# Kernel tuning notes

Measured on AMD Instinct MI355X. Metric: run time of the kernel, lower is better.

## Reference

```python
import jax, jax.numpy as jnp
import numpy as np

B, S, D, H, DH = 4, 2048, 1024, 16, 64

def setup_inputs() -> dict:
    key = jax.random.key(0)
    k1, k2, k3, k4, k5 = jax.random.split(key, 5)
    scale = 1.0 / np.sqrt(D)
    return {
        "x": jax.random.normal(k1, (B, S, D), dtype=jnp.float32),
        "w_qkv": jax.random.normal(k2, (D, 3, H, DH), dtype=jnp.float32) * scale,
        "b_qkv": jax.random.normal(k3, (3, H, DH), dtype=jnp.float32) * 0.02,
        "w_out": jax.random.normal(k4, (H, DH, D), dtype=jnp.float32) * (1.0 / np.sqrt(H * DH)),
        "b_out": jax.random.normal(k5, (D,), dtype=jnp.float32) * 0.02,
    }

def reference(x, w_qkv, b_qkv, w_out, b_out):
    # QKV projection: [B,S,D] x [D,3,H,Dh] -> [B,S,3,H,Dh]
    qkv = jnp.einsum('bsd,dthe->bsthe', x, w_qkv) + b_qkv
    q, k, v = qkv[:, :, 0], qkv[:, :, 1], qkv[:, :, 2]  # each [B,S,H,Dh]
    head_dim = q.shape[-1]
    # scores [B,H,Sq,Sk]
    scores = jnp.einsum('bqhe,bkhe->bhqk', q, k) / jnp.sqrt(jnp.float32(head_dim))
    seq = scores.shape[-1]
    causal = (jnp.arange(seq)[:, None] >= jnp.arange(seq)[None, :]).astype(scores.dtype)
    scores = scores - 1e9 * (1.0 - causal)  # additive mask as in source
    weights = jax.nn.softmax(scores, axis=-1)
    # dropout inactive (inference=True default)
    answers = jnp.einsum('bhqk,bkhe->bqhe', weights, v)  # [B,S,H,Dh]
    out = jnp.einsum('bqhe,hed->bqd', answers, w_out) + b_out
    return out
```

## Files before the change

kernel.cpp:

```cpp
#include <hip/hip_runtime.h>
#include <hip/hip_bf16.h>
#include <stdint.h>

#define B_    4
#define S_    2048
#define D_    1024
#define H_    16
#define DH_   64
#define M_TOT 8192
#define NQKV  3072
#define HDH   1024

typedef __bf16 bf16_t;
typedef bf16_t bf16x8 __attribute__((ext_vector_type(8)));
typedef float  f32x4  __attribute__((ext_vector_type(4)));
typedef float  f32x16 __attribute__((ext_vector_type(16)));

#define QSCALE 0.1803368801111204f

__device__ __forceinline__ short f2bf(float f) {
  union { float f; uint32_t u; } x; x.f = f;
  uint32_t r = (x.u + 0x7fffu + ((x.u >> 16) & 1u)) >> 16;
  return (short)(uint16_t)r;
}

__device__ __forceinline__ uint32_t cvt_pk_bf16(float lo, float hi) {
  uint32_t r;
  asm("v_cvt_pk_bf16_f32 %0, %1, %2" : "=v"(r) : "v"(lo), "v"(hi));
  return r;
}

__device__ __forceinline__ void permlane32_swap(uint32_t& d, uint32_t& s) {
  asm("v_permlane32_swap_b32 %0, %1" : "+v"(d), "+v"(s));
}

#define ASYNC_COPY16(g, l) \
  __builtin_amdgcn_global_load_lds((const __attribute__((address_space(1))) void*)(g), \
                                   (__attribute__((address_space(3))) void*)(l), 16, 0, 0)


__global__ __launch_bounds__(256) void k_cvt(const float* __restrict__ in, short* __restrict__ out, int n4) {
  int i = blockIdx.x * 256 + threadIdx.x;
  if (i < n4) {
    float4 v = ((const float4*)in)[i];
    short4 o;
    o.x = f2bf(v.x); o.y = f2bf(v.y); o.z = f2bf(v.z); o.w = f2bf(v.w);
    ((short4*)out)[i] = o;
  }
}

__global__ __launch_bounds__(256) void k_transpose_t(const float* __restrict__ in, short* __restrict__ out,
                                                     int R, int C) {
  __shared__ short t[32][33];
  const int bx = blockIdx.x * 32;
  const int by = blockIdx.y * 32;
  const int tid = threadIdx.x;
  const int row = tid >> 3, c4 = (tid & 7) * 4;
  const float4 v = *(const float4*)&in[(size_t)(by + row) * C + bx + c4];
  t[row][c4 + 0] = f2bf(v.x); t[row][c4 + 1] = f2bf(v.y);
  t[row][c4 + 2] = f2bf(v.z); t[row][c4 + 3] = f2bf(v.w);
  __syncthreads();
  short4 o;
  o.x = t[c4 + 0][row]; o.y = t[c4 + 1][row];
  o.z = t[c4 + 2][row]; o.w = t[c4 + 3][row];
  *(short4*)&out[(size_t)(bx + row) * R + by + c4] = o;
}


__device__ __forceinline__ void gemm_core(const short* __restrict__ A,
                                          const short* __restrict__ Bt,
                                          int row0, int col0, int K,
                                          short* lA, short* lB,
                                          f32x4 acc[4][4]) {
  const int tid  = threadIdx.x;
  const int wave = tid >> 6, lane = tid & 63;
  const int wr = wave >> 1, wc = wave & 1;
  const int stg_r = lane >> 2;
  const int stg_k = (lane & 3) * 8;
  const int fr = lane & 15;
  const int fk = (lane >> 4) * 8;

  for (int k0 = 0; k0 < K; k0 += 32) {
    __syncthreads();
#pragma unroll
    for (int c = 0; c < 2; ++c) {
      const int seg = wave * 2 + c;
      const short* ga = A  + (size_t)(row0 + seg * 16 + stg_r) * K + (k0 + stg_k);
      const short* gb = Bt + (size_t)(col0 + seg * 16 + stg_r) * K + (k0 + stg_k);
      ASYNC_COPY16(ga, lA + seg * 512);
      ASYNC_COPY16(gb, lB + seg * 512);
    }
    __syncthreads();
    bf16x8 af[4], bfr[4];
#pragma unroll
    for (int m = 0; m < 4; ++m)
      af[m] = *(const bf16x8*)(lA + (wr * 64 + m * 16 + fr) * 32 + fk);
#pragma unroll
    for (int n = 0; n < 4; ++n)
      bfr[n] = *(const bf16x8*)(lB + (wc * 64 + n * 16 + fr) * 32 + fk);
#pragma unroll
    for (int m = 0; m < 4; ++m)
#pragma unroll
      for (int n = 0; n < 4; ++n)
        acc[m][n] = __builtin_amdgcn_mfma_f32_16x16x32_bf16(af[m], bfr[n], acc[m][n], 0, 0, 0);
  }
}

__global__ __launch_bounds__(256) void k_gemm_qkv(const short* __restrict__ A, const short* __restrict__ Bt,
                                                  const float* __restrict__ bias,
                                                  short* __restrict__ Qb, short* __restrict__ Kb,
                                                  short* __restrict__ Vt) {
  __shared__ short lA[128 * 32];
  __shared__ short lB[128 * 32];
  f32x4 acc[4][4];
#pragma unroll
  for (int m = 0; m < 4; ++m)
#pragma unroll
    for (int n = 0; n < 4; ++n)
      acc[m][n] = (f32x4){0.f, 0.f, 0.f, 0.f};
  const int row0 = blockIdx.x * 128, col0 = blockIdx.y * 128;
  gemm_core(A, Bt, row0, col0, D_, lA, lB, acc);
  const int lane = threadIdx.x & 63, wave = threadIdx.x >> 6;
  const int wr = wave >> 1, wc = wave & 1;
#pragma unroll
  for (int m = 0; m < 4; ++m) {
    const int rbase = row0 + wr * 64 + m * 16 + (lane >> 4) * 4;
    const int bb = rbase >> 11, s0 = rbase & 2047;
#pragma unroll
    for (int n = 0; n < 4; ++n) {
      const int col = col0 + wc * 64 + n * 16 + (lane & 15);
      const float bv = bias[col];
      const int t = col >> 10, rem = col & 1023, hh = rem >> 6, e = rem & 63;
      if (t == 2) {
        short4 o;
        o.x = f2bf(acc[m][n][0] + bv);
        o.y = f2bf(acc[m][n][1] + bv);
        o.z = f2bf(acc[m][n][2] + bv);
        o.w = f2bf(acc[m][n][3] + bv);
        *(short4*)&Vt[((size_t)(bb * H_ + hh) * DH_ + e) * S_ + s0] = o;
      } else if (t == 0) {
#pragma unroll
        for (int r = 0; r < 4; ++r)
          Qb[((size_t)(bb * H_ + hh) * S_ + (s0 + r)) * DH_ + e] = f2bf((acc[m][n][r] + bv) * QSCALE);
      } else {
#pragma unroll
        for (int r = 0; r < 4; ++r)
          Kb[((size_t)(bb * H_ + hh) * S_ + (s0 + r)) * DH_ + e] = f2bf(acc[m][n][r] + bv);
      }
    }
  }
}

__global__ __launch_bounds__(256) void k_gemm_out(const short* __restrict__ A, const short* __restrict__ Bt,
                                                  const float* __restrict__ bias, float* __restrict__ C) {
  __shared__ short lA[128 * 32];
  __shared__ short lB[128 * 32];
  f32x4 acc[4][4];
#pragma unroll
  for (int m = 0; m < 4; ++m)
#pragma unroll
    for (int n = 0; n < 4; ++n)
      acc[m][n] = (f32x4){0.f, 0.f, 0.f, 0.f};
  const int row0 = blockIdx.x * 128, col0 = blockIdx.y * 128;
  gemm_core(A, Bt, row0, col0, HDH, lA, lB, acc);
  const int lane = threadIdx.x & 63, wave = threadIdx.x >> 6;
  const int wr = wave >> 1, wc = wave & 1;
#pragma unroll
  for (int m = 0; m < 4; ++m) {
    const int rbase = row0 + wr * 64 + m * 16 + (lane >> 4) * 4;
#pragma unroll
    for (int n = 0; n < 4; ++n) {
      const int col = col0 + wc * 64 + n * 16 + (lane & 15);
      const float bv = bias[col];
#pragma unroll
      for (int r = 0; r < 4; ++r)
        C[(size_t)(rbase + r) * D_ + col] = acc[m][n][r] + bv;
    }
  }
}


template <bool MASKED>
__device__ __forceinline__ void softmax_pack(const f32x16& sacc, int ql, int hi,
                                             f32x16& o0, f32x16& o1,
                                             float& m, float& lsum,
                                             bf16x8& pb0v, bf16x8& pb1v) {
  float p[16];
#pragma unroll
  for (int r = 0; r < 16; ++r) {
    float s = sacc[r];
    if (MASKED) {
      const int kl = (r & 3) + 8 * (r >> 2) + 4 * hi;
      s = (kl <= ql) ? s : -1.0e30f;
    }
    p[r] = s;
  }
  float t0 = fmaxf(fmaxf(p[0], p[1]), p[2]);
  float t1 = fmaxf(fmaxf(p[3], p[4]), p[5]);
  float t2 = fmaxf(fmaxf(p[6], p[7]), p[8]);
  float t3 = fmaxf(fmaxf(p[9], p[10]), p[11]);
  float t4 = fmaxf(fmaxf(p[12], p[13]), p[14]);
  float pmax = fmaxf(fmaxf(fmaxf(t0, t1), t2), fmaxf(fmaxf(t3, t4), p[15]));
  if (__any(pmax - m > 8.0f)) {
    const float pmr = fmaxf(pmax, __shfl_xor(pmax, 32));
    const float mn = fmaxf(m, pmr);
    const float al = __builtin_amdgcn_exp2f(m - mn);
    lsum *= al;
#pragma unroll
    for (int r = 0; r < 16; ++r) { o0[r] *= al; o1[r] *= al; }
    m = mn;
  }
#pragma unroll
  for (int r = 0; r < 16; ++r) p[r] = __builtin_amdgcn_exp2f(p[r] - m);
  {
    float s0 = (p[0] + p[1]) + (p[2] + p[3]);
    float s1 = (p[4] + p[5]) + (p[6] + p[7]);
    float s2 = (p[8] + p[9]) + (p[10] + p[11]);
    float s3 = (p[12] + p[13]) + (p[14] + p[15]);
    lsum += (s0 + s1) + (s2 + s3);
  }
  uint32_t A0 = cvt_pk_bf16(p[0],  p[1]);
  uint32_t A1 = cvt_pk_bf16(p[2],  p[3]);
  uint32_t B0 = cvt_pk_bf16(p[4],  p[5]);
  uint32_t B1 = cvt_pk_bf16(p[6],  p[7]);
  uint32_t A2 = cvt_pk_bf16(p[8],  p[9]);
  uint32_t A3 = cvt_pk_bf16(p[10], p[11]);
  uint32_t B2 = cvt_pk_bf16(p[12], p[13]);
  uint32_t B3 = cvt_pk_bf16(p[14], p[15]);
  permlane32_swap(A0, B0);
  permlane32_swap(A1, B1);
  permlane32_swap(A2, B2);
  permlane32_swap(A3, B3);
  union { uint32_t u[4]; bf16x8 v; } pb0, pb1;
  pb0.u[0] = A0; pb0.u[1] = A1; pb0.u[2] = B0; pb0.u[3] = B1;
  pb1.u[0] = A2; pb1.u[1] = A3; pb1.u[2] = B2; pb1.u[3] = B3;
  pb0v = pb0.v; pb1v = pb1.v;
}

template <bool MASKED>
__device__ __forceinline__ void attn_tile(int kt, int ql, int hi,
                                          const short* __restrict__ Kp,
                                          const short* __restrict__ Vp,
                                          const bf16x8 qf[4],
                                          f32x16& oacc0, f32x16& oacc1,
                                          float& m, float& lsum) {
  const short* kb = Kp + (size_t)(kt + ql) * DH_ + hi * 8;
  bf16x8 kf0 = *(const bf16x8*)(kb);
  bf16x8 kf1 = *(const bf16x8*)(kb + 16);
  bf16x8 kf2 = *(const bf16x8*)(kb + 32);
  bf16x8 kf3 = *(const bf16x8*)(kb + 48);
  const short* vb0 = Vp + (size_t)(ql) * S_ + kt + hi * 8;
  const short* vb1 = Vp + (size_t)(32 + ql) * S_ + kt + hi * 8;
  bf16x8 vf00 = *(const bf16x8*)(vb0);
  bf16x8 vf01 = *(const bf16x8*)(vb0 + 16);
  bf16x8 vf10 = *(const bf16x8*)(vb1);
  bf16x8 vf11 = *(const bf16x8*)(vb1 + 16);

  f32x16 sacc;
#pragma unroll
  for (int r = 0; r < 16; ++r) sacc[r] = 0.f;
  __builtin_amdgcn_s_setprio(1);
  sacc = __builtin_amdgcn_mfma_f32_32x32x16_bf16(kf0, qf[0], sacc, 0, 0, 0);
  sacc = __builtin_amdgcn_mfma_f32_32x32x16_bf16(kf1, qf[1], sacc, 0, 0, 0);
  sacc = __builtin_amdgcn_mfma_f32_32x32x16_bf16(kf2, qf[2], sacc, 0, 0, 0);
  sacc = __builtin_amdgcn_mfma_f32_32x32x16_bf16(kf3, qf[3], sacc, 0, 0, 0);
  __builtin_amdgcn_s_setprio(0);

  bf16x8 pb0, pb1;
  softmax_pack<MASKED>(sacc, ql, hi, oacc0, oacc1, m, lsum, pb0, pb1);

  __builtin_amdgcn_s_setprio(1);
  oacc0 = __builtin_amdgcn_mfma_f32_32x32x16_bf16(vf00, pb0, oacc0, 0, 0, 0);
  oacc0 = __builtin_amdgcn_mfma_f32_32x32x16_bf16(vf01, pb1, oacc0, 0, 0, 0);
  oacc1 = __builtin_amdgcn_mfma_f32_32x32x16_bf16(vf10, pb0, oacc1, 0, 0, 0);
  oacc1 = __builtin_amdgcn_mfma_f32_32x32x16_bf16(vf11, pb1, oacc1, 0, 0, 0);
  __builtin_amdgcn_s_setprio(0);
}

template <bool MASKA>
__device__ __forceinline__ void attn_tile2(int kt, int ql, int hi,
                                           const short* __restrict__ Kp,
                                           const short* __restrict__ Vp,
                                           const bf16x8 qfA[4], const bf16x8 qfB[4],
                                           f32x16& oA0, f32x16& oA1, float& mA, float& lA,
                                           f32x16& oB0, f32x16& oB1, float& mB, float& lB) {
  const short* kb = Kp + (size_t)(kt + ql) * DH_ + hi * 8;
  bf16x8 kf0 = *(const bf16x8*)(kb);
  bf16x8 kf1 = *(const bf16x8*)(kb + 16);
  bf16x8 kf2 = *(const bf16x8*)(kb + 32);
  bf16x8 kf3 = *(const bf16x8*)(kb + 48);
  const short* vb0 = Vp + (size_t)(ql) * S_ + kt + hi * 8;
  const short* vb1 = Vp + (size_t)(32 + ql) * S_ + kt + hi * 8;
  bf16x8 vf00 = *(const bf16x8*)(vb0);
  bf16x8 vf01 = *(const bf16x8*)(vb0 + 16);
  bf16x8 vf10 = *(const bf16x8*)(vb1);
  bf16x8 vf11 = *(const bf16x8*)(vb1 + 16);

  f32x16 sA, sB;
#pragma unroll
  for (int r = 0; r < 16; ++r) { sA[r] = 0.f; sB[r] = 0.f; }
  __builtin_amdgcn_s_setprio(1);
  sA = __builtin_amdgcn_mfma_f32_32x32x16_bf16(kf0, qfA[0], sA, 0, 0, 0);
  sB = __builtin_amdgcn_mfma_f32_32x32x16_bf16(kf0, qfB[0], sB, 0, 0, 0);
  sA = __builtin_amdgcn_mfma_f32_32x32x16_bf16(kf1, qfA[1], sA, 0, 0, 0);
  sB = __builtin_amdgcn_mfma_f32_32x32x16_bf16(kf1, qfB[1], sB, 0, 0, 0);
  sA = __builtin_amdgcn_mfma_f32_32x32x16_bf16(kf2, qfA[2], sA, 0, 0, 0);
  sB = __builtin_amdgcn_mfma_f32_32x32x16_bf16(kf2, qfB[2], sB, 0, 0, 0);
  sA = __builtin_amdgcn_mfma_f32_32x32x16_bf16(kf3, qfA[3], sA, 0, 0, 0);
  sB = __builtin_amdgcn_mfma_f32_32x32x16_bf16(kf3, qfB[3], sB, 0, 0, 0);
  __builtin_amdgcn_s_setprio(0);

  bf16x8 pA0, pA1, pB0, pB1;
  softmax_pack<MASKA>(sA, ql, hi, oA0, oA1, mA, lA, pA0, pA1);
  softmax_pack<false>(sB, ql, hi, oB0, oB1, mB, lB, pB0, pB1);

  __builtin_amdgcn_s_setprio(1);
  oA0 = __builtin_amdgcn_mfma_f32_32x32x16_bf16(vf00, pA0, oA0, 0, 0, 0);
  oB0 = __builtin_amdgcn_mfma_f32_32x32x16_bf16(vf00, pB0, oB0, 0, 0, 0);
  oA0 = __builtin_amdgcn_mfma_f32_32x32x16_bf16(vf01, pA1, oA0, 0, 0, 0);
  oB0 = __builtin_amdgcn_mfma_f32_32x32x16_bf16(vf01, pB1, oB0, 0, 0, 0);
  oA1 = __builtin_amdgcn_mfma_f32_32x32x16_bf16(vf10, pA0, oA1, 0, 0, 0);
  oB1 = __builtin_amdgcn_mfma_f32_32x32x16_bf16(vf10, pB0, oB1, 0, 0, 0);
  oA1 = __builtin_amdgcn_mfma_f32_32x32x16_bf16(vf11, pA1, oA1, 0, 0, 0);
  oB1 = __builtin_amdgcn_mfma_f32_32x32x16_bf16(vf11, pB1, oB1, 0, 0, 0);
  __builtin_amdgcn_s_setprio(0);
}

__device__ __forceinline__ void write_out(short* __restrict__ att, int b, int h,
                                          int q0, int ql, int hi,
                                          const f32x16& o0, const f32x16& o1, float lsum) {
  lsum += __shfl_xor(lsum, 32);
  const float rl = __builtin_amdgcn_rcpf(lsum);
  short* ob = att + (size_t)((size_t)b * S_ + q0 + ql) * HDH + h * DH_ + 4 * hi;
#pragma unroll
  for (int dt = 0; dt < 2; ++dt) {
#pragma unroll
    for (int a = 0; a < 4; ++a) {
      const int rb = 4 * a;
      float v0 = (dt ? o1[rb + 0] : o0[rb + 0]) * rl;
      float v1 = (dt ? o1[rb + 1] : o0[rb + 1]) * rl;
      float v2 = (dt ? o1[rb + 2] : o0[rb + 2]) * rl;
      float v3 = (dt ? o1[rb + 3] : o0[rb + 3]) * rl;
      short4 o;
      o.x = f2bf(v0); o.y = f2bf(v1); o.z = f2bf(v2); o.w = f2bf(v3);
      *(short4*)(ob + dt * 32 + 8 * a) = o;
    }
  }
}

__global__ __launch_bounds__(64, 3) void k_attn(const short* __restrict__ Qb, const short* __restrict__ Kb,
                                                const short* __restrict__ Vt, short* __restrict__ att) {
  const int lane = threadIdx.x & 63;
  const int j = blockIdx.x;
  const int xcd = j & 7, c = j >> 3;
  const int bhLo = c & 7;
  const int s = 31 - (c >> 3);
  const int gg = xcd + 8 * bhLo;
  const int b = gg >> 4, h = gg & 15;
  const int pA = 2 * s, pB = 2 * s + 1;
  const int qA = pA * 32, qB = pB * 32;
  const size_t bh = (size_t)(b * H_ + h);
  const short* Qp = Qb + bh * (S_ * DH_);
  const short* Kp = Kb + bh * (S_ * DH_);
  const short* Vp = Vt + bh * (DH_ * S_);
  const int ql = lane & 31, hi = lane >> 5;

  bf16x8 qfA[4], qfB[4];
#pragma unroll
  for (int ss = 0; ss < 4; ++ss) {
    qfA[ss] = *(const bf16x8*)(Qp + (size_t)(qA + ql) * DH_ + ss * 16 + hi * 8);
    qfB[ss] = *(const bf16x8*)(Qp + (size_t)(qB + ql) * DH_ + ss * 16 + hi * 8);
  }

  f32x16 oA0, oA1, oB0, oB1;
#pragma unroll
  for (int r = 0; r < 16; ++r) { oA0[r] = 0.f; oA1[r] = 0.f; oB0[r] = 0.f; oB1[r] = 0.f; }
  float mA = -3.0e38f, lA = 0.f, mB = -3.0e38f, lB = 0.f;

#pragma unroll 1
  for (int t = 0; t < pA; ++t)
    attn_tile2<false>(t * 32, ql, hi, Kp, Vp, qfA, qfB, oA0, oA1, mA, lA, oB0, oB1, mB, lB);
  attn_tile2<true>(qA, ql, hi, Kp, Vp, qfA, qfB, oA0, oA1, mA, lA, oB0, oB1, mB, lB);
  attn_tile<true>(qB, ql, hi, Kp, Vp, qfB, oB0, oB1, mB, lB);

  write_out(att, b, h, qA, ql, hi, oA0, oA1, lA);
  write_out(att, b, h, qB, ql, hi, oB0, oB1, lB);
}


extern "C" void kernel_launch(void* const* d_in, const int* in_sizes, int n_in,
                              void* d_out, int out_size, void* d_ws, size_t ws_size,
                              hipStream_t stream) {
  const float* x     = (const float*)d_in[0];
  const float* w_qkv = (const float*)d_in[1];
  const float* b_qkv = (const float*)d_in[2];
  const float* w_out = (const float*)d_in[3];
  const float* b_out = (const float*)d_in[4];
  float* out = (float*)d_out;

  char* p = (char*)d_ws;
  short* xb    = (short*)p; p += (size_t)M_TOT * D_ * 2;
  short* wqkvT = (short*)p; p += (size_t)NQKV * D_ * 2;
  short* woutT = (short*)p; p += (size_t)D_ * HDH * 2;
  short* Qb    = (short*)p; p += (size_t)B_ * H_ * S_ * DH_ * 2;
  short* Kb    = (short*)p; p += (size_t)B_ * H_ * S_ * DH_ * 2;
  short* Vt    = (short*)p; p += (size_t)B_ * H_ * S_ * DH_ * 2;
  short* att   = (short*)p; p += (size_t)M_TOT * HDH * 2;

  k_cvt<<<M_TOT * D_ / 4 / 256, 256, 0, stream>>>(x, xb, M_TOT * D_ / 4);
  k_transpose_t<<<dim3(NQKV / 32, D_ / 32), 256, 0, stream>>>(w_qkv, wqkvT, D_, NQKV);
  k_transpose_t<<<dim3(D_ / 32, HDH / 32), 256, 0, stream>>>(w_out, woutT, HDH, D_);
  k_gemm_qkv<<<dim3(M_TOT / 128, NQKV / 128), 256, 0, stream>>>(xb, wqkvT, b_qkv, Qb, Kb, Vt);
  k_attn<<<2048, 64, 0, stream>>>(Qb, Kb, Vt, att);
  k_gemm_out<<<dim3(M_TOT / 128, D_ / 128), 256, 0, stream>>>(att, woutT, b_out, out);
}
```

Before: 199.0 us.

## Split attention KV range across two workgroups and merge partials in a new kernel

Each causal query-pair's KV loop is split into two halves run by separate workgroups (4096 instead of 2048). Each half writes an unnormalized bf16 partial output plus its running max and sum, and a new merge kernel combines them with log-sum-exp rescaling. The aim is better load balance and occupancy across CUs for the long causal rows. The cost is an extra kernel launch, extra global traffic for the partials, and an additional bf16 rounding of the unnormalized accumulators.

```diff
diff --git a/kernel.cpp b/kernel.cpp
--- a/kernel.cpp
+++ b/kernel.cpp
@@ -22,6 +22,10 @@
   union { float f; uint32_t u; } x; x.f = f;
   uint32_t r = (x.u + 0x7fffu + ((x.u >> 16) & 1u)) >> 16;
   return (short)(uint16_t)r;
+}
+
+__device__ __forceinline__ float bf2f(uint16_t u) {
+  union { uint32_t u; float f; } x; x.u = (uint32_t)u << 16; return x.f;
 }
 
 __device__ __forceinline__ uint32_t cvt_pk_bf16(float lo, float hi) {
@@ -326,39 +330,44 @@
   __builtin_amdgcn_s_setprio(0);
 }
 
-__device__ __forceinline__ void write_out(short* __restrict__ att, int b, int h,
-                                          int q0, int ql, int hi,
-                                          const f32x16& o0, const f32x16& o1, float lsum) {
+__device__ __forceinline__ void store_partial(short* __restrict__ Opart, float* __restrict__ Mpart,
+                                              float* __restrict__ Lpart, int idx, int ql, int hi,
+                                              const f32x16& o0, const f32x16& o1,
+                                              float m, float lsum) {
   lsum += __shfl_xor(lsum, 32);
-  const float rl = __builtin_amdgcn_rcpf(lsum);
-  short* ob = att + (size_t)((size_t)b * S_ + q0 + ql) * HDH + h * DH_ + 4 * hi;
+  short* base = Opart + (size_t)idx * 2048;
 #pragma unroll
   for (int dt = 0; dt < 2; ++dt) {
 #pragma unroll
     for (int a = 0; a < 4; ++a) {
       const int rb = 4 * a;
-      float v0 = (dt ? o1[rb + 0] : o0[rb + 0]) * rl;
-      float v1 = (dt ? o1[rb + 1] : o0[rb + 1]) * rl;
-      float v2 = (dt ? o1[rb + 2] : o0[rb + 2]) * rl;
-      float v3 = (dt ? o1[rb + 3] : o0[rb + 3]) * rl;
-      short4 o;
-      o.x = f2bf(v0); o.y = f2bf(v1); o.z = f2bf(v2); o.w = f2bf(v3);
-      *(short4*)(ob + dt * 32 + 8 * a) = o;
-    }
-  }
+      short4 v;
+      v.x = f2bf(dt ? o1[rb + 0] : o0[rb + 0]);
+      v.y = f2bf(dt ? o1[rb + 1] : o0[rb + 1]);
+      v.z = f2bf(dt ? o1[rb + 2] : o0[rb + 2]);
+      v.w = f2bf(dt ? o1[rb + 3] : o0[rb + 3]);
+      *(short4*)&base[(dt * 4 + a) * 256 + (hi * 32 + ql) * 4] = v;
+    }
+  }
+  if (hi == 0) { Mpart[idx * 32 + ql] = m; Lpart[idx * 32 + ql] = lsum; }
 }
 
 __global__ __launch_bounds__(64, 3) void k_attn(const short* __restrict__ Qb, const short* __restrict__ Kb,
-                                                const short* __restrict__ Vt, short* __restrict__ att) {
+                                                const short* __restrict__ Vt,
+                                                short* __restrict__ Opart, float* __restrict__ Mpart,
+                                                float* __restrict__ Lpart) {
   const int lane = threadIdx.x & 63;
   const int j = blockIdx.x;
   const int xcd = j & 7, c = j >> 3;
-  const int bhLo = c & 7;
-  const int s = 31 - (c >> 3);
+  const int half = c & 1, r = c >> 1;
+  const int bhLo = r & 7;
+  const int s = 31 - (r >> 3);
   const int gg = xcd + 8 * bhLo;
   const int b = gg >> 4, h = gg & 15;
+  const int pairId = gg * 32 + s;
   const int pA = 2 * s, pB = 2 * s + 1;
   const int qA = pA * 32, qB = pB * 32;
+  const int c0 = (s + 1 < pA) ? (s + 1) : pA;
   const size_t bh = (size_t)(b * H_ + h);
   const short* Qp = Qb + bh * (S_ * DH_);
   const short* Kp = Kb + bh * (S_ * DH_);
@@ -374,17 +383,64 @@
 
   f32x16 oA0, oA1, oB0, oB1;
 #pragma unroll
-  for (int r = 0; r < 16; ++r) { oA0[r] = 0.f; oA1[r] = 0.f; oB0[r] = 0.f; oB1[r] = 0.f; }
+  for (int rr = 0; rr < 16; ++rr) { oA0[rr] = 0.f; oA1[rr] = 0.f; oB0[rr] = 0.f; oB1[rr] = 0.f; }
   float mA = -3.0e38f, lA = 0.f, mB = -3.0e38f, lB = 0.f;
 
+  if (half == 0) {
 #pragma unroll 1
-  for (int t = 0; t < pA; ++t)
-    attn_tile2<false>(t * 32, ql, hi, Kp, Vp, qfA, qfB, oA0, oA1, mA, lA, oB0, oB1, mB, lB);
-  attn_tile2<true>(qA, ql, hi, Kp, Vp, qfA, qfB, oA0, oA1, mA, lA, oB0, oB1, mB, lB);
-  attn_tile<true>(qB, ql, hi, Kp, Vp, qfB, oB0, oB1, mB, lB);
-
-  write_out(att, b, h, qA, ql, hi, oA0, oA1, lA);
-  write_out(att, b, h, qB, ql, hi, oB0, oB1, lB);
+    for (int t = 0; t < c0; ++t)
+      attn_tile2<false>(t * 32, ql, hi, Kp, Vp, qfA, qfB, oA0, oA1, mA, lA, oB0, oB1, mB, lB);
+  } else {
+#pragma unroll 1
+    for (int t = c0; t < pA; ++t)
+      attn_tile2<false>(t * 32, ql, hi, Kp, Vp, qfA, qfB, oA0, oA1, mA, lA, oB0, oB1, mB, lB);
+    attn_tile2<true>(qA, ql, hi, Kp, Vp, qfA, qfB, oA0, oA1, mA, lA, oB0, oB1, mB, lB);
+    attn_tile<true>(qB, ql, hi, Kp, Vp, qfB, oB0, oB1, mB, lB);
+  }
+
+  store_partial(Opart, Mpart, Lpart, (pairId * 2 + 0) * 2 + half, ql, hi, oA0, oA1, mA, lA);
+  store_partial(Opart, Mpart, Lpart, (pairId * 2 + 1) * 2 + half, ql, hi, oB0, oB1, mB, lB);
+}
+
+__global__ __launch_bounds__(64) void k_merge(const short* __restrict__ Opart,
+                                              const float* __restrict__ Mpart,
+                                              const float* __restrict__ Lpart,
+                                              short* __restrict__ att) {
+  const int u = blockIdx.x;
+  const int pairId = u >> 1, st = u & 1;
+  const int gg = pairId >> 5, s = pairId & 31;
+  const int b = gg >> 4, h = gg & 15;
+  const int q0 = (2 * s + st) * 32;
+  const int lane = threadIdx.x & 63;
+  const int ql = lane & 31, hi = lane >> 5;
+  const int idx0 = u * 2, idx1 = u * 2 + 1;
+
+  const float m0 = Mpart[idx0 * 32 + ql], m1 = Mpart[idx1 * 32 + ql];
+  const float M = fmaxf(m0, m1);
+  const float a0 = __builtin_amdgcn_exp2f(m0 - M);
+  const float a1 = __builtin_amdgcn_exp2f(m1 - M);
+  const float L = Lpart[idx0 * 32 + ql] * a0 + Lpart[idx1 * 32 + ql] * a1;
+  const float rL = __builtin_amdgcn_rcpf(L);
+  const float f0 = a0 * rL, f1 = a1 * rL;
+
+  const short* b0 = Opart + (size_t)idx0 * 2048;
+  const short* b1 = Opart + (size_t)idx1 * 2048;
+  short* ob = att + (size_t)((size_t)b * S_ + q0 + ql) * HDH + h * DH_ + 4 * hi;
+#pragma unroll
+  for (int dt = 0; dt < 2; ++dt) {
+#pragma unroll
+    for (int a = 0; a < 4; ++a) {
+      const int off = (dt * 4 + a) * 256 + (hi * 32 + ql) * 4;
+      short4 x0 = *(const short4*)&b0[off];
+      short4 x1 = *(const short4*)&b1[off];
+      short4 w;
+      w.x = f2bf(bf2f((uint16_t)x0.x) * f0 + bf2f((uint16_t)x1.x) * f1);
+      w.y = f2bf(bf2f((uint16_t)x0.y) * f0 + bf2f((uint16_t)x1.y) * f1);
+      w.z = f2bf(bf2f((uint16_t)x0.z) * f0 + bf2f((uint16_t)x1.z) * f1);
+      w.w = f2bf(bf2f((uint16_t)x0.w) * f0 + bf2f((uint16_t)x1.w) * f1);
+      *(short4*)(ob + dt * 32 + 8 * a) = w;
+    }
+  }
 }
 
 
@@ -406,11 +462,15 @@
   short* Kb    = (short*)p; p += (size_t)B_ * H_ * S_ * DH_ * 2;
   short* Vt    = (short*)p; p += (size_t)B_ * H_ * S_ * DH_ * 2;
   short* att   = (short*)p; p += (size_t)M_TOT * HDH * 2;
+  short* Opart = (short*)p; p += (size_t)8192 * 2048 * 2;
+  float* Mpart = (float*)p; p += (size_t)8192 * 32 * 4;
+  float* Lpart = (float*)p; p += (size_t)8192 * 32 * 4;
 
   k_cvt<<<M_TOT * D_ / 4 / 256, 256, 0, stream>>>(x, xb, M_TOT * D_ / 4);
   k_transpose_t<<<dim3(NQKV / 32, D_ / 32), 256, 0, stream>>>(w_qkv, wqkvT, D_, NQKV);
   k_transpose_t<<<dim3(D_ / 32, HDH / 32), 256, 0, stream>>>(w_out, woutT, HDH, D_);
   k_gemm_qkv<<<dim3(M_TOT / 128, NQKV / 128), 256, 0, stream>>>(xb, wqkvT, b_qkv, Qb, Kb, Vt);
-  k_attn<<<2048, 64, 0, stream>>>(Qb, Kb, Vt, att);
+  k_attn<<<4096, 64, 0, stream>>>(Qb, Kb, Vt, Opart, Mpart, Lpart);
+  k_merge<<<4096, 64, 0, stream>>>(Opart, Mpart, Lpart, att);
   k_gemm_out<<<dim3(M_TOT / 128, D_ / 128), 256, 0, stream>>>(att, woutT, b_out, out);
 }
```

Result: slower. 226.2 us (+13.7%).
